# Performance work log

Hardware: AMD Instinct MI355X
Metric: run time of the kernel (lower is better)

The kernel has to match this reference:

```python
import jax, jax.numpy as jnp
import numpy as np

N_NODES = 100000

def _gcn_layer(x, W, b, src, dst, n):
    # x: [N, Fin], W: [Fin, Fout], b: [Fout]; edges src->dst, [E]
    h = x @ W  # [N, Fout]
    # add self loops
    loops = jnp.arange(n, dtype=src.dtype)
    s = jnp.concatenate([src, loops])
    d = jnp.concatenate([dst, loops])
    # symmetric GCN normalization: deg^{-1/2}[s] * deg^{-1/2}[d]
    deg = jax.ops.segment_sum(jnp.ones_like(d, dtype=h.dtype), d, num_segments=n)
    dis = jnp.where(deg > 0, jax.lax.rsqrt(jnp.maximum(deg, 1.0)), 0.0)
    norm = dis[s] * dis[d]  # [E+N]
    msg = h[s] * norm[:, None]  # [E+N, Fout]
    out = jax.ops.segment_sum(msg, d, num_segments=n)  # [N, Fout]
    return out + b


def setup_inputs() -> dict:
    key = jax.random.key(0)
    k1, k2, k3, k4, k5 = jax.random.split(key, 5)
    in_feat, hidden, out_feat = 64, 128, 64
    n_edges = 1600000
    node_features = jax.random.normal(k1, (N_NODES, in_feat), dtype=jnp.float32)
    edge_index = jax.random.randint(k2, (2, n_edges), 0, N_NODES, dtype=jnp.int32)
    # glorot-ish params
    W1 = jax.random.normal(k3, (in_feat, hidden), dtype=jnp.float32) * (1.0 / np.sqrt(in_feat))
    b1 = jnp.zeros((hidden,), dtype=jnp.float32)
    W2 = jax.random.normal(k4, (hidden, out_feat), dtype=jnp.float32) * (1.0 / np.sqrt(hidden))
    b2 = jnp.zeros((out_feat,), dtype=jnp.float32)
    return {"node_features": node_features, "edge_index": edge_index,
            "W1": W1, "b1": b1, "W2": W2, "b2": b2}


def reference(node_features, edge_index, W1, b1, W2, b2):
    src, dst = edge_index[0], edge_index[1]
    n = node_features.shape[0]
    h = _gcn_layer(node_features, W1, b1, src, dst, n)
    h = jax.nn.relu(h)
    h = _gcn_layer(h, W2, b2, src, dst, n)
    return h
```

## Files before the change

kernel.cpp:

```cpp
#include <hip/hip_runtime.h>
#include <hip/hip_fp16.h>

#define NN 100000
#define NB 391
#define NG 256
#define REGION 6144

using f16x8 = __attribute__((ext_vector_type(8))) _Float16;
using f32x4 = __attribute__((ext_vector_type(4))) float;

__global__ __launch_bounds__(256) void bhist_kernel(const int* __restrict__ dst,
                                                    int* __restrict__ counts, int E) {
    __shared__ int h[NB];
    for (int i = threadIdx.x; i < NB; i += 256) h[i] = 0;
    __syncthreads();
    const int chunk = (E + NG - 1) / NG;
    const int lo = blockIdx.x * chunk, hi = min(E, lo + chunk);
    for (int e = lo + threadIdx.x; e < hi; e += 256) atomicAdd(&h[dst[e] >> 8], 1);
    __syncthreads();
    for (int i = threadIdx.x; i < NB; i += 256) counts[i * NG + blockIdx.x] = h[i];
}

__global__ __launch_bounds__(256) void bprefix_kernel(int* __restrict__ counts,
                                                      int* __restrict__ btot,
                                                      const float* __restrict__ W1,
                                                      const float* __restrict__ W2,
                                                      __half* __restrict__ W1t,
                                                      __half* __restrict__ W2t) {
    const int b = blockIdx.x, t = threadIdx.x;
    if (b == NB) {
        for (int i = t; i < 64 * 128; i += 256) {
            int k = i / 128, c = i % 128;
            W1t[c * 64 + k] = __float2half(W1[i]);
            int k2 = i / 64, c2 = i % 64;
            W2t[c2 * 128 + k2] = __float2half(W2[i]);
        }
        return;
    }
    __shared__ int sm[256];
    int v = counts[b * NG + t];
    sm[t] = v; __syncthreads();
    for (int off = 1; off < 256; off <<= 1) {
        int x = (t >= off) ? sm[t - off] : 0; __syncthreads();
        sm[t] += x; __syncthreads();
    }
    counts[b * NG + t] = b * REGION + sm[t] - v;
    if (t == 255) btot[b] = sm[255];
}

__global__ __launch_bounds__(256) void bscatter_kernel(const int* __restrict__ src,
                                                       const int* __restrict__ dst,
                                                       const int* __restrict__ cstart,
                                                       int* __restrict__ staging, int E) {
    __shared__ int cur[NB];
    for (int i = threadIdx.x; i < NB; i += 256) cur[i] = cstart[i * NG + blockIdx.x];
    __syncthreads();
    const int chunk = (E + NG - 1) / NG;
    const int lo = blockIdx.x * chunk, hi = min(E, lo + chunk);
    for (int e = lo + threadIdx.x; e < hi; e += 256) {
        int d = dst[e];
        int pos = atomicAdd(&cur[d >> 8], 1);
        staging[pos] = src[e] | ((d & 255) << 17);
    }
}

__global__ __launch_bounds__(256) void bfinal_kernel(const int* __restrict__ btot,
                                                     const int* __restrict__ staging,
                                                     int* __restrict__ csr,
                                                     int* __restrict__ row_beg,
                                                     int* __restrict__ row_end,
                                                     float* __restrict__ dis,
                                                     const float* __restrict__ x,
                                                     __half* __restrict__ xh,
                                                     int N) {
    __shared__ int h[256];
    __shared__ int sc[256];
    __shared__ int cur[256];
    __shared__ float sdis[256];
    const int b = blockIdx.x, t = threadIdx.x;
    const int base = b * REGION;
    const int endb = base + btot[b];
    h[t] = 0; __syncthreads();
    for (int i = base + t; i < endb; i += 256) atomicAdd(&h[staging[i] >> 17], 1);
    __syncthreads();
    int v = h[t];
    sc[t] = v; __syncthreads();
    for (int off = 1; off < 256; off <<= 1) {
        int xv = (t >= off) ? sc[t - off] : 0; __syncthreads();
        sc[t] += xv; __syncthreads();
    }
    int excl = sc[t] - v;
    cur[t] = base + excl;
    float dv = rsqrtf((float)v + 1.0f);
    sdis[t] = dv;
    int node = b * 256 + t;
    if (node < N) {
        row_beg[node] = base + excl;
        row_end[node] = base + excl + v;
        dis[node] = dv;
    }
    __syncthreads();
    for (int i = base + t; i < endb; i += 256) {
        int p = staging[i];
        int pos = atomicAdd(&cur[p >> 17], 1);
        csr[pos] = p & 0x1FFFF;
    }
    const int node0 = b * 256;
    const int nmax = min(256, N - node0);
    for (int i = t; i < nmax * 16; i += 256) {
        int nl = i >> 4, c4 = i & 15;
        float4 vx = ((const float4*)x)[(size_t)(node0 + nl) * 16 + c4];
        float wq = sdis[nl];
        __half2* o = (__half2*)&xh[(size_t)(node0 + nl) * 64 + c4 * 4];
        o[0] = __floats2half2_rn(vx.x * wq, vx.y * wq);
        o[1] = __floats2half2_rn(vx.z * wq, vx.w * wq);
    }
}

__global__ __launch_bounds__(256) void gatherG1_kernel(const __half* __restrict__ tab,
                                                       const float* __restrict__ dis,
                                                       const __half* __restrict__ W1t,
                                                       const float* __restrict__ b1,
                                                       const int* __restrict__ row_beg,
                                                       const int* __restrict__ row_end,
                                                       const int* __restrict__ csr,
                                                       __half* __restrict__ h1h, int N,
                                                       float one) {
    __shared__ _Float16 sA[16][72];
    const int tid = threadIdx.x;
    const int nodeL = tid >> 4;
    const int node = blockIdx.x * 16 + nodeL;
    const int l16 = tid & 15;
    const int e = l16 >> 3;
    const int sub = l16 & 7;
    const int beg = row_beg[node], end = row_end[node];

    float acc[8];
    if (e == 0) {
        f16x8 sv = *reinterpret_cast<const f16x8*>(&tab[(size_t)node * 64 + sub * 8]);
        #pragma unroll
        for (int q = 0; q < 8; ++q) acc[q] = (float)sv[q];
    } else {
        #pragma unroll
        for (int q = 0; q < 8; ++q) acc[q] = 0.0f;
    }
    for (int j = beg + e; j < end; j += 2) {
        int s = csr[j];
        f16x8 v = *reinterpret_cast<const f16x8*>(&tab[(size_t)s * 64 + sub * 8]);
        #pragma unroll
        for (int q = 0; q < 8; ++q) acc[q] = fmaf((float)v[q], one, acc[q]);
    }
    #pragma unroll
    for (int q = 0; q < 8; ++q) acc[q] += __shfl_xor(acc[q], 8);

    if (e == 0) {
        const float dd = dis[node];
        f16x8 o;
        #pragma unroll
        for (int q = 0; q < 8; ++q) o[q] = (_Float16)(acc[q] * dd);
        *reinterpret_cast<f16x8*>(&sA[nodeL][sub * 8]) = o;
    }
    __syncthreads();

    const int wid = tid >> 6, lane = tid & 63;
    const int lrow = lane & 15, kgrp = lane >> 4;
    f32x4 acc2[2];
    acc2[0] = (f32x4){0.f, 0.f, 0.f, 0.f};
    acc2[1] = (f32x4){0.f, 0.f, 0.f, 0.f};
    #pragma unroll
    for (int ks = 0; ks < 2; ++ks) {
        const int kbase = ks * 32 + kgrp * 8;
        f16x8 a = *reinterpret_cast<const f16x8*>(&sA[lrow][kbase]);
        #pragma unroll
        for (int nt = 0; nt < 2; ++nt) {
            const int col = (wid * 2 + nt) * 16 + lrow;
            f16x8 b = *reinterpret_cast<const f16x8*>(&W1t[(size_t)col * 64 + kbase]);
            acc2[nt] = __builtin_amdgcn_mfma_f32_16x16x32_f16(a, b, acc2[nt], 0, 0, 0);
        }
    }
    #pragma unroll
    for (int nt = 0; nt < 2; ++nt) {
        const int col = (wid * 2 + nt) * 16 + lrow;
        const float bb = b1[col];
        #pragma unroll
        for (int r = 0; r < 4; ++r) {
            const int row = blockIdx.x * 16 + kgrp * 4 + r;
            float v = fmaxf(acc2[nt][r] + bb, 0.0f);
            h1h[(size_t)row * 128 + col] = __float2half(v);
        }
    }
}

__global__ __launch_bounds__(256) void gemm2_kernel(const __half* __restrict__ A,
                                                    const __half* __restrict__ Wt,
                                                    const float* __restrict__ dis,
                                                    __half* __restrict__ C, int N) {
    constexpr int K = 128, F = 64;
    constexpr int NT = F / 32;
    const int wid  = threadIdx.x >> 6;
    const int lane = threadIdx.x & 63;
    const int wr = wid >> 1;
    const int wc = wid & 1;
    const int row0 = blockIdx.x * 32 + wr * 16;
    const int col0 = wc * (F / 2);
    const int lrow = lane & 15;
    const int kgrp = lane >> 4;

    f32x4 acc[NT];
    #pragma unroll
    for (int nt = 0; nt < NT; ++nt) acc[nt] = (f32x4){0.f, 0.f, 0.f, 0.f};
    #pragma unroll
    for (int ks = 0; ks < K / 32; ++ks) {
        const int kbase = ks * 32 + kgrp * 8;
        f16x8 a = *reinterpret_cast<const f16x8*>(&A[(size_t)(row0 + lrow) * K + kbase]);
        #pragma unroll
        for (int nt = 0; nt < NT; ++nt) {
            f16x8 b = *reinterpret_cast<const f16x8*>(&Wt[(size_t)(col0 + nt * 16 + lrow) * K + kbase]);
            acc[nt] = __builtin_amdgcn_mfma_f32_16x16x32_f16(a, b, acc[nt], 0, 0, 0);
        }
    }
    #pragma unroll
    for (int nt = 0; nt < NT; ++nt) {
        const int col = col0 + nt * 16 + lrow;
        #pragma unroll
        for (int r = 0; r < 4; ++r) {
            const int row = row0 + kgrp * 4 + r;
            C[(size_t)row * F + col] = __float2half(acc[nt][r] * dis[row]);
        }
    }
}

__global__ __launch_bounds__(256) void gather2_kernel(const __half* __restrict__ tab,
                                                      const float* __restrict__ dis,
                                                      const float* __restrict__ b,
                                                      const int* __restrict__ row_beg,
                                                      const int* __restrict__ row_end,
                                                      const int* __restrict__ csr,
                                                      float* __restrict__ out, int N,
                                                      float one) {
    const int node = blockIdx.x * 4 + (threadIdx.x >> 6);
    const int lane = threadIdx.x & 63;
    const int g   = lane >> 3;
    const int sub = lane & 7;
    if (node >= N) return;
    const int beg = row_beg[node], end = row_end[node];

    float acc[8];
    {
        f16x8 sv = *reinterpret_cast<const f16x8*>(&tab[(size_t)node * 64 + sub * 8]);
        #pragma unroll
        for (int q = 0; q < 8; ++q) acc[q] = (g == 0) ? (float)sv[q] : 0.0f;
    }
    int j = beg;
    for (; j + 16 <= end; j += 16) {
        int sA = csr[j + g];
        int sB = csr[j + 8 + g];
        f16x8 vA = *reinterpret_cast<const f16x8*>(&tab[(size_t)sA * 64 + sub * 8]);
        f16x8 vB = *reinterpret_cast<const f16x8*>(&tab[(size_t)sB * 64 + sub * 8]);
        #pragma unroll
        for (int q = 0; q < 8; ++q) acc[q] = fmaf((float)vA[q], one, acc[q]);
        #pragma unroll
        for (int q = 0; q < 8; ++q) acc[q] = fmaf((float)vB[q], one, acc[q]);
    }
    if (j + 8 <= end) {
        int s = csr[j + g];
        f16x8 v = *reinterpret_cast<const f16x8*>(&tab[(size_t)s * 64 + sub * 8]);
        #pragma unroll
        for (int q = 0; q < 8; ++q) acc[q] = fmaf((float)v[q], one, acc[q]);
        j += 8;
    }
    if (j + g < end) {
        int s = csr[j + g];
        f16x8 v = *reinterpret_cast<const f16x8*>(&tab[(size_t)s * 64 + sub * 8]);
        #pragma unroll
        for (int q = 0; q < 8; ++q) acc[q] = fmaf((float)v[q], one, acc[q]);
    }
    #pragma unroll
    for (int q = 0; q < 8; ++q) {
        acc[q] += __shfl_xor(acc[q], 8);
        acc[q] += __shfl_xor(acc[q], 16);
        acc[q] += __shfl_xor(acc[q], 32);
    }
    if (g == 0) {
        const float dd = dis[node];
        float vv[8];
        #pragma unroll
        for (int q = 0; q < 8; ++q) vv[q] = acc[q] * dd + b[sub * 8 + q];
        float* op = &out[(size_t)node * 64 + sub * 8];
        *reinterpret_cast<float4*>(op)     = make_float4(vv[0], vv[1], vv[2], vv[3]);
        *reinterpret_cast<float4*>(op + 4) = make_float4(vv[4], vv[5], vv[6], vv[7]);
    }
}

extern "C" void kernel_launch(void* const* d_in, const int* in_sizes, int n_in,
                              void* d_out, int out_size, void* d_ws, size_t ws_size,
                              hipStream_t stream) {
    const float* x  = (const float*)d_in[0];
    const int*   ei = (const int*)d_in[1];
    const float* W1 = (const float*)d_in[2];
    const float* b1 = (const float*)d_in[3];
    const float* W2 = (const float*)d_in[4];
    const float* b2 = (const float*)d_in[5];
    float* out = (float*)d_out;

    const int N = NN;
    const int E = in_sizes[1] / 2;
    const int* src = ei;
    const int* dst = ei + E;

    int* counts   = (int*)d_ws;
    int* btot     = counts + NB * NG;
    int* row_beg  = btot + 512;
    int* row_end  = row_beg + N;
    float* dis    = (float*)(row_end + N);
    int* staging  = (int*)(dis + N);
    int* csr      = staging + (size_t)NB * REGION;
    float* base   = (float*)(csr + (size_t)NB * REGION);
    __half* xh    = (__half*)base;
    __half* zh    = (__half*)(base + (size_t)N * 32);
    __half* h1h   = (__half*)(base + (size_t)N * 64);
    __half* W1t   = (__half*)(base + (size_t)N * 128);
    __half* W2t   = W1t + 128 * 64;

    bhist_kernel<<<NG, 256, 0, stream>>>(dst, counts, E);
    bprefix_kernel<<<NB + 1, 256, 0, stream>>>(counts, btot, W1, W2, W1t, W2t);
    bscatter_kernel<<<NG, 256, 0, stream>>>(src, dst, counts, staging, E);
    bfinal_kernel<<<NB, 256, 0, stream>>>(btot, staging, csr, row_beg, row_end, dis, x, xh, N);

    gatherG1_kernel<<<N / 16, 256, 0, stream>>>(xh, dis, W1t, b1, row_beg, row_end, csr, h1h, N, 1.0f);

    gemm2_kernel<<<N / 32, 256, 0, stream>>>(h1h, W2t, dis, zh, N);
    gather2_kernel<<<N / 4, 256, 0, stream>>>(zh, dis, b2, row_beg, row_end, csr, out, N, 1.0f);
}
```

Before: 182.1 us.

## Fuse layer-1 gather, both GEMMs into one kernel; double histogram groups

The layer-1 aggregation, the W1 GEMM with ReLU, and the W2 GEMM with dis scaling now run in one 512-thread kernel. The hidden activations stay in shared memory and are never written to or read back from global memory. Each node gets 4 edge-parallel lanes instead of 2, and the K=128 second GEMM is split across 8 waves with a shared-memory reduction. The bucket-sort histogram uses 512 edge groups with a group-major count layout, and each prefix thread scans two entries; this adds partitioning work but gives more parallelism in the scatter passes.

Result: faster. 166.3 us (-8.6%).

```diff
diff --git a/kernel.cpp b/kernel.cpp
--- a/kernel.cpp
+++ b/kernel.cpp
@@ -3,7 +3,7 @@
 
 #define NN 100000
 #define NB 391
-#define NG 256
+#define NG 512
 #define REGION 6144
 
 using f16x8 = __attribute__((ext_vector_type(8))) _Float16;
@@ -14,11 +14,12 @@
     __shared__ int h[NB];
     for (int i = threadIdx.x; i < NB; i += 256) h[i] = 0;
     __syncthreads();
+    const int g = blockIdx.x;
     const int chunk = (E + NG - 1) / NG;
-    const int lo = blockIdx.x * chunk, hi = min(E, lo + chunk);
+    const int lo = g * chunk, hi = min(E, lo + chunk);
     for (int e = lo + threadIdx.x; e < hi; e += 256) atomicAdd(&h[dst[e] >> 8], 1);
     __syncthreads();
-    for (int i = threadIdx.x; i < NB; i += 256) counts[i * NG + blockIdx.x] = h[i];
+    for (int i = threadIdx.x; i < NB; i += 256) counts[g * NB + i] = h[i];
 }
 
 __global__ __launch_bounds__(256) void bprefix_kernel(int* __restrict__ counts,
@@ -38,13 +39,25 @@
         return;
     }
     __shared__ int sm[256];
-    int v = counts[b * NG + t];
-    sm[t] = v; __syncthreads();
+    int loc[NG / 256];
+    int s = 0;
+    #pragma unroll
+    for (int p = 0; p < NG / 256; ++p) {
+        loc[p] = counts[((NG / 256) * t + p) * NB + b];
+        s += loc[p];
+    }
+    sm[t] = s; __syncthreads();
     for (int off = 1; off < 256; off <<= 1) {
         int x = (t >= off) ? sm[t - off] : 0; __syncthreads();
         sm[t] += x; __syncthreads();
     }
-    counts[b * NG + t] = b * REGION + sm[t] - v;
+    int run = b * REGION + sm[t] - s;
+    #pragma unroll
+    for (int p = 0; p < NG / 256; ++p) {
+        int c = loc[p];
+        counts[((NG / 256) * t + p) * NB + b] = run;
+        run += c;
+    }
     if (t == 255) btot[b] = sm[255];
 }
 
@@ -53,10 +66,11 @@
                                                        const int* __restrict__ cstart,
                                                        int* __restrict__ staging, int E) {
     __shared__ int cur[NB];
-    for (int i = threadIdx.x; i < NB; i += 256) cur[i] = cstart[i * NG + blockIdx.x];
+    const int g = blockIdx.x;
+    for (int i = threadIdx.x; i < NB; i += 256) cur[i] = cstart[g * NB + i];
     __syncthreads();
     const int chunk = (E + NG - 1) / NG;
-    const int lo = blockIdx.x * chunk, hi = min(E, lo + chunk);
+    const int lo = g * chunk, hi = min(E, lo + chunk);
     for (int e = lo + threadIdx.x; e < hi; e += 256) {
         int d = dst[e];
         int pos = atomicAdd(&cur[d >> 8], 1);
@@ -117,42 +131,45 @@
     }
 }
 
-__global__ __launch_bounds__(256) void gatherG1_kernel(const __half* __restrict__ tab,
-                                                       const float* __restrict__ dis,
-                                                       const __half* __restrict__ W1t,
-                                                       const float* __restrict__ b1,
-                                                       const int* __restrict__ row_beg,
-                                                       const int* __restrict__ row_end,
-                                                       const int* __restrict__ csr,
-                                                       __half* __restrict__ h1h, int N,
-                                                       float one) {
+__global__ __launch_bounds__(512) void gfuse_kernel(const __half* __restrict__ tab,
+                                                    const float* __restrict__ dis,
+                                                    const __half* __restrict__ W1t,
+                                                    const float* __restrict__ b1,
+                                                    const __half* __restrict__ W2t,
+                                                    const int* __restrict__ row_beg,
+                                                    const int* __restrict__ row_end,
+                                                    const int* __restrict__ csr,
+                                                    __half* __restrict__ zh, int N,
+                                                    float one) {
     __shared__ _Float16 sA[16][72];
+    __shared__ _Float16 sH[16][136];
+    __shared__ float sP[4][16][16];
     const int tid = threadIdx.x;
-    const int nodeL = tid >> 4;
-    const int node = blockIdx.x * 16 + nodeL;
-    const int l16 = tid & 15;
-    const int e = l16 >> 3;
-    const int sub = l16 & 7;
+    const int nodeL = tid >> 5;
+    const int l32 = tid & 31;
+    const int e = l32 >> 3;
+    const int sub = l32 & 7;
+    const int node0 = blockIdx.x * 16;
+    const int node = node0 + nodeL;
     const int beg = row_beg[node], end = row_end[node];
 
     float acc[8];
-    if (e == 0) {
+    {
         f16x8 sv = *reinterpret_cast<const f16x8*>(&tab[(size_t)node * 64 + sub * 8]);
         #pragma unroll
-        for (int q = 0; q < 8; ++q) acc[q] = (float)sv[q];
-    } else {
-        #pragma unroll
-        for (int q = 0; q < 8; ++q) acc[q] = 0.0f;
-    }
-    for (int j = beg + e; j < end; j += 2) {
+        for (int q = 0; q < 8; ++q) acc[q] = (e == 0) ? (float)sv[q] : 0.0f;
+    }
+    for (int j = beg + e; j < end; j += 4) {
         int s = csr[j];
         f16x8 v = *reinterpret_cast<const f16x8*>(&tab[(size_t)s * 64 + sub * 8]);
         #pragma unroll
         for (int q = 0; q < 8; ++q) acc[q] = fmaf((float)v[q], one, acc[q]);
     }
     #pragma unroll
-    for (int q = 0; q < 8; ++q) acc[q] += __shfl_xor(acc[q], 8);
-
+    for (int q = 0; q < 8; ++q) {
+        acc[q] += __shfl_xor(acc[q], 8);
+        acc[q] += __shfl_xor(acc[q], 16);
+    }
     if (e == 0) {
         const float dd = dis[node];
         f16x8 o;
@@ -162,70 +179,49 @@
     }
     __syncthreads();
 
-    const int wid = tid >> 6, lane = tid & 63;
+    const int w = tid >> 6, lane = tid & 63;
     const int lrow = lane & 15, kgrp = lane >> 4;
-    f32x4 acc2[2];
-    acc2[0] = (f32x4){0.f, 0.f, 0.f, 0.f};
-    acc2[1] = (f32x4){0.f, 0.f, 0.f, 0.f};
-    #pragma unroll
-    for (int ks = 0; ks < 2; ++ks) {
-        const int kbase = ks * 32 + kgrp * 8;
-        f16x8 a = *reinterpret_cast<const f16x8*>(&sA[lrow][kbase]);
-        #pragma unroll
-        for (int nt = 0; nt < 2; ++nt) {
-            const int col = (wid * 2 + nt) * 16 + lrow;
-            f16x8 b = *reinterpret_cast<const f16x8*>(&W1t[(size_t)col * 64 + kbase]);
-            acc2[nt] = __builtin_amdgcn_mfma_f32_16x16x32_f16(a, b, acc2[nt], 0, 0, 0);
-        }
-    }
-    #pragma unroll
-    for (int nt = 0; nt < 2; ++nt) {
-        const int col = (wid * 2 + nt) * 16 + lrow;
+    {
+        const int col = w * 16 + lrow;
+        f32x4 a1 = (f32x4){0.f, 0.f, 0.f, 0.f};
+        #pragma unroll
+        for (int ks = 0; ks < 2; ++ks) {
+            const int kbase = ks * 32 + kgrp * 8;
+            f16x8 a  = *reinterpret_cast<const f16x8*>(&sA[lrow][kbase]);
+            f16x8 bf = *reinterpret_cast<const f16x8*>(&W1t[(size_t)col * 64 + kbase]);
+            a1 = __builtin_amdgcn_mfma_f32_16x16x32_f16(a, bf, a1, 0, 0, 0);
+        }
         const float bb = b1[col];
         #pragma unroll
         for (int r = 0; r < 4; ++r) {
-            const int row = blockIdx.x * 16 + kgrp * 4 + r;
-            float v = fmaxf(acc2[nt][r] + bb, 0.0f);
-            h1h[(size_t)row * 128 + col] = __float2half(v);
-        }
-    }
-}
-
-__global__ __launch_bounds__(256) void gemm2_kernel(const __half* __restrict__ A,
-                                                    const __half* __restrict__ Wt,
-                                                    const float* __restrict__ dis,
-                                                    __half* __restrict__ C, int N) {
-    constexpr int K = 128, F = 64;
-    constexpr int NT = F / 32;
-    const int wid  = threadIdx.x >> 6;
-    const int lane = threadIdx.x & 63;
-    const int wr = wid >> 1;
-    const int wc = wid & 1;
-    const int row0 = blockIdx.x * 32 + wr * 16;
-    const int col0 = wc * (F / 2);
-    const int lrow = lane & 15;
-    const int kgrp = lane >> 4;
-
-    f32x4 acc[NT];
-    #pragma unroll
-    for (int nt = 0; nt < NT; ++nt) acc[nt] = (f32x4){0.f, 0.f, 0.f, 0.f};
-    #pragma unroll
-    for (int ks = 0; ks < K / 32; ++ks) {
-        const int kbase = ks * 32 + kgrp * 8;
-        f16x8 a = *reinterpret_cast<const f16x8*>(&A[(size_t)(row0 + lrow) * K + kbase]);
-        #pragma unroll
-        for (int nt = 0; nt < NT; ++nt) {
-            f16x8 b = *reinterpret_cast<const f16x8*>(&Wt[(size_t)(col0 + nt * 16 + lrow) * K + kbase]);
-            acc[nt] = __builtin_amdgcn_mfma_f32_16x16x32_f16(a, b, acc[nt], 0, 0, 0);
-        }
-    }
-    #pragma unroll
-    for (int nt = 0; nt < NT; ++nt) {
-        const int col = col0 + nt * 16 + lrow;
-        #pragma unroll
-        for (int r = 0; r < 4; ++r) {
-            const int row = row0 + kgrp * 4 + r;
-            C[(size_t)row * F + col] = __float2half(acc[nt][r] * dis[row]);
+            const int row = kgrp * 4 + r;
+            sH[row][col] = (_Float16)fmaxf(a1[r] + bb, 0.0f);
+        }
+    }
+    __syncthreads();
+    {
+        const int t2 = w & 3, kh = w >> 2;
+        const int col = t2 * 16 + lrow;
+        f32x4 a2 = (f32x4){0.f, 0.f, 0.f, 0.f};
+        #pragma unroll
+        for (int ks = 0; ks < 2; ++ks) {
+            const int kbase = kh * 64 + ks * 32 + kgrp * 8;
+            f16x8 a  = *reinterpret_cast<const f16x8*>(&sH[lrow][kbase]);
+            f16x8 bf = *reinterpret_cast<const f16x8*>(&W2t[(size_t)col * 128 + kbase]);
+            a2 = __builtin_amdgcn_mfma_f32_16x16x32_f16(a, bf, a2, 0, 0, 0);
+        }
+        if (kh == 1) {
+            #pragma unroll
+            for (int r = 0; r < 4; ++r) sP[t2][kgrp * 4 + r][lrow] = a2[r];
+        }
+        __syncthreads();
+        if (kh == 0) {
+            #pragma unroll
+            for (int r = 0; r < 4; ++r) {
+                const int row = kgrp * 4 + r;
+                float v = (a2[r] + sP[t2][row][lrow]) * dis[node0 + row];
+                zh[(size_t)(node0 + row) * 64 + col] = __float2half(v);
+            }
         }
     }
 }
@@ -309,7 +305,7 @@
     const int* dst = ei + E;
 
     int* counts   = (int*)d_ws;
-    int* btot     = counts + NB * NG;
+    int* btot     = counts + NG * NB;
     int* row_beg  = btot + 512;
     int* row_end  = row_beg + N;
     float* dis    = (float*)(row_end + N);
@@ -318,8 +314,7 @@
     float* base   = (float*)(csr + (size_t)NB * REGION);
     __half* xh    = (__half*)base;
     __half* zh    = (__half*)(base + (size_t)N * 32);
-    __half* h1h   = (__half*)(base + (size_t)N * 64);
-    __half* W1t   = (__half*)(base + (size_t)N * 128);
+    __half* W1t   = (__half*)(base + (size_t)N * 64);
     __half* W2t   = W1t + 128 * 64;
 
     bhist_kernel<<<NG, 256, 0, stream>>>(dst, counts, E);
@@ -327,8 +322,7 @@
     bscatter_kernel<<<NG, 256, 0, stream>>>(src, dst, counts, staging, E);
     bfinal_kernel<<<NB, 256, 0, stream>>>(btot, staging, csr, row_beg, row_end, dis, x, xh, N);
 
-    gatherG1_kernel<<<N / 16, 256, 0, stream>>>(xh, dis, W1t, b1, row_beg, row_end, csr, h1h, N, 1.0f);
-
-    gemm2_kernel<<<N / 32, 256, 0, stream>>>(h1h, W2t, dis, zh, N);
+    gfuse_kernel<<<N / 16, 512, 0, stream>>>(xh, dis, W1t, b1, W2t, row_beg, row_end, csr, zh, N, 1.0f);
+
     gather2_kernel<<<N / 4, 256, 0, stream>>>(zh, dis, b2, row_beg, row_end, csr, out, N, 1.0f);
 }
```
